# Kernel tuning notes

Measured on AMD Instinct MI355X. Metric: run time of the kernel, lower is better.

## Reference

```python
import jax, jax.numpy as jnp
import numpy as np

N_GRAPHS = 512
NODES_PER_G = 200
EDGES_PER_G = 6400
N = N_GRAPHS * NODES_PER_G        # 102400 nodes
E = N_GRAPHS * EDGES_PER_G        # 3276800 edges
HID = 128
NCLS = 10


def _linear_params(key, fan_in, fan_out):
    # torch nn.Linear default init: U(-1/sqrt(fan_in), 1/sqrt(fan_in))
    s = 1.0 / np.sqrt(fan_in)
    kw, kb = jax.random.split(key)
    W = jax.random.uniform(kw, (fan_in, fan_out), minval=-s, maxval=s, dtype=jnp.float32)
    b = jax.random.uniform(kb, (fan_out,), minval=-s, maxval=s, dtype=jnp.float32)
    return W, b


def setup_inputs() -> dict:
    key = jax.random.key(0)
    ks = jax.random.split(key, 10)
    # edges are confined within each graph (DGL batched graph structure)
    g_off = (jnp.arange(E, dtype=jnp.int32) // EDGES_PER_G) * NODES_PER_G
    src = (g_off + jax.random.randint(ks[0], (E,), 0, NODES_PER_G)).astype(jnp.int32)
    dst = (g_off + jax.random.randint(ks[1], (E,), 0, NODES_PER_G)).astype(jnp.int32)
    W1, b1 = _linear_params(ks[2], 1, HID)
    W2, b2 = _linear_params(ks[3], HID, HID)
    Wa, ba = _linear_params(ks[4], HID, 512)
    Wb, bb = _linear_params(ks[5], 512, 1024)
    Wc, bc = _linear_params(ks[6], 1024, 1024)
    Wd, bd = _linear_params(ks[7], 1024, 512)
    We, be = _linear_params(ks[8], 512, NCLS)
    return dict(src=src, dst=dst, W1=W1, b1=b1, W2=W2, b2=b2,
                Wa=Wa, ba=ba, Wb=Wb, bb=bb, Wc=Wc, bc=bc,
                Wd=Wd, bd=bd, We=We, be=be)


def reference(src, dst, W1, b1, W2, b2, Wa, ba, Wb, bb, Wc, bc, Wd, bd, We, be):
    seg = jax.ops.segment_sum
    ones = jnp.ones((E,), jnp.float32)
    in_deg = seg(ones, dst, num_segments=N)    # [N]
    out_deg = seg(ones, src, num_segments=N)   # [N]
    # DGL GraphConv norm='both': degrees clamped to min 1
    inv_out = (1.0 / jnp.sqrt(jnp.maximum(out_deg, 1.0)))[:, None]
    inv_in = (1.0 / jnp.sqrt(jnp.maximum(in_deg, 1.0)))[:, None]

    def gconv(h, W, b):
        h = (h @ W) * inv_out                    # src-side normalize (weight applied first; same math)
        h = seg(h[src], dst, num_segments=N)     # gather + scatter-add aggregation
        return h * inv_in + b                    # dst-side normalize + bias

    h = in_deg[:, None]                          # input node features = in-degrees, [N,1]
    h = jax.nn.relu(gconv(h, W1, b1))
    h = jax.nn.relu(gconv(h, W2, b2))

    gid = jnp.arange(N, dtype=jnp.int32) // NODES_PER_G
    hg = seg(h, gid, num_segments=N_GRAPHS) / float(NODES_PER_G)  # mean readout, [G,HID]

    x = jax.nn.relu(hg @ Wa + ba)
    x = jax.nn.relu(x @ Wb + bb)
    x = jax.nn.relu(x @ Wc + bc)
    x = jax.nn.relu(x @ Wd + bd)
    return jax.nn.softmax(x @ We + be, axis=-1)  # nn.Softmax over class dim
```

## Files before the change

kernel.cpp:

```cpp
#include <hip/hip_runtime.h>
#include <stdint.h>

typedef unsigned short u16;
typedef unsigned int   u32;

#define NG   512
#define NPG  200
#define EPG  6400
#define NN   (NG*NPG)
#define NE_  (NG*EPG)
#define HID  128
#define KP   224
#define AP   232
#define ZP   136
#define RQ   64
#define QCAP 2048

__device__ __forceinline__ float bf2f(u16 b){ u32 u = ((u32)b) << 16; return __builtin_bit_cast(float, u); }
__device__ __forceinline__ u16 f2bf(float f){
    u32 u = __builtin_bit_cast(u32, f);
    u = (u + 0x7FFFu + ((u >> 16) & 1u)) >> 16;
    return (u16)u;
}

typedef __attribute__((ext_vector_type(8))) short bf16x8;
typedef __attribute__((ext_vector_type(4))) float f32x4;

enum : int {
  O_W1 = 0,        O_b1 = 128,      O_W2 = 256,      O_b2 = 16640,
  O_Wa = 16768,    O_ba = 82304,    O_Wb = 82816,    O_bb = 607104,
  O_Wc = 608128,   O_bc = 1656704,  O_Wd = 1657728,  O_bd = 2182016,
  O_We = 2182528,  O_be = 2187648,  O_END = 2187658
};

enum : int {
  T_Wa = 0,
  T_Wb = 65536,
  T_Wc = 65536 + 524288,
  T_Wd = 65536 + 524288 + 1048576,
  T_END = 65536 + 524288 + 1048576 + 524288
};

__global__ __launch_bounds__(128) void k_detect(const u16* __restrict__ w1bits,
                                                int* __restrict__ flag)
{
    __shared__ int cnt;
    const int tid = threadIdx.x;
    if (tid == 0) cnt = 0;
    __syncthreads();
    u16 u = w1bits[tid];
    int e = (u >> 7) & 0xFF;
    if (e >= 0x7F) atomicAdd(&cnt, 1);
    __syncthreads();
    if (tid == 0) *flag = (cnt > 4) ? 1 : 0;
}

struct Cvt { const void* src[14]; int off[15]; };

__global__ __launch_bounds__(256) void k_convert(Cvt c, float* __restrict__ dst,
                                                 const int* __restrict__ flag, int total)
{
    const int f = *flag;
    int i = blockIdx.x * 256 + threadIdx.x;
    if (i >= total) return;
    int t = 0;
    while (i >= c.off[t+1]) t++;
    int j = i - c.off[t];
    dst[i] = f ? ((const float*)c.src[t])[j] : bf2f(((const u16*)c.src[t])[j]);
}

__global__ __launch_bounds__(256) void k_w2t(const void* __restrict__ w2src,
                                             const float* __restrict__ w2canon,
                                             u16* __restrict__ W2T,
                                             float* __restrict__ hg,
                                             const int* __restrict__ flag)
{
    int i = blockIdx.x * 256 + threadIdx.x;
    if (i < HID*HID){
        int outc = i >> 7, inc = i & 127;
        int jsrc = inc*HID + outc;
        W2T[i] = (*flag) ? f2bf(w2canon[jsrc]) : ((const u16*)w2src)[jsrc];
    }
    #pragma unroll
    for (int k = 0; k < 4; k++){
        int j = blockIdx.x * 1024 + k*256 + threadIdx.x;
        if (j < NG*HID) hg[j] = 0.f;
    }
}

struct TD { const void* src; int coff; int logK; int N; int dst0; int dst1; };
struct TD4 { TD t[4]; };

__global__ __launch_bounds__(256) void k_wt(TD4 d, const float* __restrict__ canon,
                                            u16* __restrict__ dst,
                                            const int* __restrict__ flag, int total)
{
    const int f = *flag;
    int i = blockIdx.x * 256 + threadIdx.x;
    if (i >= total) return;
    int t = 0;
    while (i >= d.t[t].dst1) t++;
    const TD& td = d.t[t];
    int j = i - td.dst0;
    int n = j >> td.logK;
    int k = j & ((1 << td.logK) - 1);
    int srcidx = k * td.N + n;
    dst[i] = f ? f2bf(canon[td.coff + srcidx]) : ((const u16*)td.src)[srcidx];
}

__global__ __launch_bounds__(256) void k_graph_l1(
    const int* __restrict__ src, const int* __restrict__ dst,
    const float* __restrict__ W1, const float* __restrict__ b1,
    float* __restrict__ invInG, u16* __restrict__ h1sT,
    u32* __restrict__ edgeBuf, int* __restrict__ cntQ)
{
    __shared__ u16 srcL[EPG];
    __shared__ u16 dstL[EPG];
    __shared__ int degIn[NPG];
    __shared__ int degOut[NPG];
    __shared__ int qcur[4];
    __shared__ float sValL[NPG], sAgg[NPG], iiL[NPG], ioL[NPG], tL[NPG];
    __shared__ float w1L[HID], b1L[HID];

    const int g = blockIdx.x, tid = threadIdx.x;

    if (tid < NPG){ degIn[tid] = 0; degOut[tid] = 0; sAgg[tid] = 0.f; }
    if (tid < HID){ w1L[tid] = W1[tid]; b1L[tid] = b1[tid]; }
    if (tid < 4) qcur[tid] = 0;
    __syncthreads();

    const int ebase = g * EPG;
    #pragma unroll
    for (int i = 0; i < EPG/256; i++){
        int e = i*256 + tid;
        int s = src[ebase + e] - g*NPG;
        int d = dst[ebase + e] - g*NPG;
        srcL[e] = (u16)s; dstL[e] = (u16)d;
        atomicAdd(&degOut[s], 1);
        atomicAdd(&degIn[d], 1);
    }
    __syncthreads();

    if (tid < NPG){
        int din = degIn[tid], dout = degOut[tid];
        float ii = rsqrtf(fmaxf((float)din, 1.f));
        float io = rsqrtf(fmaxf((float)dout, 1.f));
        iiL[tid] = ii; ioL[tid] = io;
        sValL[tid] = (float)din * io;
        invInG[g*NPG + tid] = ii;
    }
    __syncthreads();

    #pragma unroll
    for (int i = 0; i < EPG/256; i++){
        int e = i*256 + tid;
        int s = srcL[e], d = dstL[e];
        atomicAdd(&sAgg[d], sValL[s]);
        int q = (d * 41) >> 11;
        int pos = atomicAdd(&qcur[q], 1);
        if (pos < QCAP)
            edgeBuf[((size_t)(g*4 + q))*QCAP + pos] = (u32)s | ((u32)(d - q*50) << 16);
    }
    __syncthreads();

    if (tid < 4) cntQ[g*4 + tid] = (qcur[tid] < QCAP) ? qcur[tid] : QCAP;
    if (tid < NPG) tL[tid] = sAgg[tid] * iiL[tid];
    __syncthreads();

    const size_t base = (size_t)g * HID * KP;
    #pragma unroll 4
    for (int i = 0; i < HID*KP/256; i++){
        int idx = i*256 + tid;
        int c = idx / KP, v = idx - c*KP;
        u16 o = 0;
        if (v < NPG)
            o = f2bf(fmaxf(fmaf(tL[v], w1L[c], b1L[c]), 0.f) * ioL[v]);
        h1sT[base + idx] = o;
    }
}

__global__ __launch_bounds__(256, 4) void k_fused_graph(
    const u32* __restrict__ edgeBuf, const int* __restrict__ cntQ,
    const u16* __restrict__ h1sT, const u16* __restrict__ W2T,
    const float* __restrict__ invInG, const float* __restrict__ b2,
    float* __restrict__ hg)
{
    __shared__ __align__(16) u16 AZ[RQ*AP];
    __shared__ float invInL[RQ];
    __shared__ float b2L[HID];
    __shared__ float poolL[HID];

    const int bid = blockIdx.x, tid = threadIdx.x;
    const int g = bid >> 2, q = bid & 3;
    u32* az32 = (u32*)AZ;
    uint4* az4 = (uint4*)AZ;

    #pragma unroll
    for (int i = 0; i < 8; i++){
        int idx = i*256 + tid;
        if (idx < RQ*AP/8) az4[idx] = make_uint4(0,0,0,0);
    }
    if (tid < HID){ b2L[tid] = b2[tid]; poolL[tid] = 0.f; }
    if (tid < RQ) invInL[tid] = (tid < 50) ? invInG[g*NPG + q*50 + tid] : 0.f;
    __syncthreads();

    const int cnt = cntQ[bid];
    const u32* eb = edgeBuf + (size_t)bid * QCAP;
    for (int i = tid; i < cnt; i += 256){
        u32 e = eb[i];
        int s = e & 0xFFFF, dl = e >> 16;
        int idx = dl*AP + s;
        atomicAdd(&az32[idx >> 1], 1u << (16*(idx & 1)));
    }
    __syncthreads();

    for (int i = tid; i < RQ*AP/2; i += 256){
        u32 wv = az32[i];
        if (wv)
            az32[i] = (u32)f2bf((float)(wv & 0xFFFFu)) | ((u32)f2bf((float)(wv >> 16)) << 16);
    }
    __syncthreads();

    const int w = tid >> 6, lane = tid & 63;
    const int wm = w >> 1, wn = w & 1;
    const int lr = lane & 15, quad = lane >> 4;

    f32x4 acc[2][4];
    const f32x4 fz = {0.f, 0.f, 0.f, 0.f};
    #pragma unroll
    for (int mi = 0; mi < 2; mi++)
        #pragma unroll
        for (int nt = 0; nt < 4; nt++) acc[mi][nt] = fz;

    {
        const u16* Bg = h1sT + (size_t)g * HID * KP + (size_t)(wn*64) * KP;
        bf16x8 bcur[4], bnxt[4];
        #pragma unroll
        for (int nt = 0; nt < 4; nt++)
            bcur[nt] = *(const bf16x8*)&Bg[(nt*16 + lr)*KP + quad*8];
        for (int ks = 0; ks < 7; ks++){
            if (ks < 6){
                #pragma unroll
                for (int nt = 0; nt < 4; nt++)
                    bnxt[nt] = *(const bf16x8*)&Bg[(nt*16 + lr)*KP + (ks+1)*32 + quad*8];
            }
            bf16x8 af[2];
            #pragma unroll
            for (int mi = 0; mi < 2; mi++)
                af[mi] = *(const bf16x8*)&AZ[((wm*2 + mi)*16 + lr)*AP + ks*32 + quad*8];
            #pragma unroll
            for (int mi = 0; mi < 2; mi++)
                #pragma unroll
                for (int nt = 0; nt < 4; nt++)
                    acc[mi][nt] = __builtin_amdgcn_mfma_f32_16x16x32_bf16(
                        af[mi], bcur[nt], acc[mi][nt], 0, 0, 0);
            #pragma unroll
            for (int nt = 0; nt < 4; nt++) bcur[nt] = bnxt[nt];
        }
    }
    __syncthreads();

    #pragma unroll
    for (int mi = 0; mi < 2; mi++)
        #pragma unroll
        for (int nt = 0; nt < 4; nt++)
            #pragma unroll
            for (int r = 0; r < 4; r++){
                int v = (wm*2 + mi)*16 + quad*4 + r;
                int c = wn*64 + nt*16 + lr;
                AZ[v*ZP + c] = f2bf(acc[mi][nt][r]);
            }
    __syncthreads();

    #pragma unroll
    for (int mi = 0; mi < 2; mi++)
        #pragma unroll
        for (int nt = 0; nt < 4; nt++) acc[mi][nt] = fz;
    {
        const u16* Wg = W2T + (size_t)(wn*64) * HID;
        bf16x8 bcur[4], bnxt[4];
        #pragma unroll
        for (int nt = 0; nt < 4; nt++)
            bcur[nt] = *(const bf16x8*)&Wg[(nt*16 + lr)*HID + quad*8];
        for (int ks = 0; ks < 4; ks++){
            if (ks < 3){
                #pragma unroll
                for (int nt = 0; nt < 4; nt++)
                    bnxt[nt] = *(const bf16x8*)&Wg[(nt*16 + lr)*HID + (ks+1)*32 + quad*8];
            }
            bf16x8 af[2];
            #pragma unroll
            for (int mi = 0; mi < 2; mi++)
                af[mi] = *(const bf16x8*)&AZ[((wm*2 + mi)*16 + lr)*ZP + ks*32 + quad*8];
            #pragma unroll
            for (int mi = 0; mi < 2; mi++)
                #pragma unroll
                for (int nt = 0; nt < 4; nt++)
                    acc[mi][nt] = __builtin_amdgcn_mfma_f32_16x16x32_bf16(
                        af[mi], bcur[nt], acc[mi][nt], 0, 0, 0);
            #pragma unroll
            for (int nt = 0; nt < 4; nt++) bcur[nt] = bnxt[nt];
        }
    }

    #pragma unroll
    for (int mi = 0; mi < 2; mi++)
        #pragma unroll
        for (int nt = 0; nt < 4; nt++){
            int c = wn*64 + nt*16 + lr;
            float s = 0.f;
            #pragma unroll
            for (int r = 0; r < 4; r++){
                int v = (wm*2 + mi)*16 + quad*4 + r;
                if (v < 50)
                    s += fmaxf(fmaf(acc[mi][nt][r], invInL[v], b2L[c]), 0.f);
            }
            atomicAdd(&poolL[c], s);
        }
    __syncthreads();
    if (tid < HID) atomicAdd(&hg[(size_t)g*HID + tid], poolL[tid] * (1.f / NPG));
}

template<int K, bool AF32>
__global__ __launch_bounds__(512) void k_mlp3(
    const void* __restrict__ Ahi_, const u16* __restrict__ Alo,
    const u16* __restrict__ WT, const float* __restrict__ bias,
    u16* __restrict__ Ohi, u16* __restrict__ Olo, int Nc)
{
    __shared__ float red[32][68];

    const int tid = threadIdx.x;
    const int w = tid >> 6, lane = tid & 63;
    const int kz = w >> 2, wm = (w >> 1) & 1, wn = w & 1;
    const int lr = lane & 15, quad = lane >> 4;
    const int row0 = blockIdx.x * 32, col0 = blockIdx.y * 64;
    const int m = row0 + wm*16 + lr;
    constexpr int KH = K / 2;
    const int k0 = kz * KH;

    const float* Af = (const float*)Ahi_;
    const u16*   Ah = (const u16*)Ahi_;

    const f32x4 fz = {0.f, 0.f, 0.f, 0.f};
    f32x4 acc[2] = {fz, fz};

    #pragma unroll
    for (int ks = 0; ks < KH/32; ks++){
        const int kk = k0 + ks*32 + quad*8;
        bf16x8 ahi, alo;
        if constexpr (AF32){
            float xs[8];
            *(float4*)&xs[0] = *(const float4*)&Af[(size_t)m*K + kk];
            *(float4*)&xs[4] = *(const float4*)&Af[(size_t)m*K + kk + 4];
            #pragma unroll
            for (int j = 0; j < 8; j++){
                u16 hh = f2bf(xs[j]);
                ahi[j] = (short)hh;
                alo[j] = (short)f2bf(xs[j] - bf2f(hh));
            }
        } else {
            ahi = *(const bf16x8*)&Ah[(size_t)m*K + kk];
            alo = *(const bf16x8*)&Alo[(size_t)m*K + kk];
        }
        #pragma unroll
        for (int nt = 0; nt < 2; nt++){
            int n = col0 + wn*32 + nt*16 + lr;
            bf16x8 b = *(const bf16x8*)&WT[(size_t)n*K + kk];
            acc[nt] = __builtin_amdgcn_mfma_f32_16x16x32_bf16(ahi, b, acc[nt], 0, 0, 0);
            acc[nt] = __builtin_amdgcn_mfma_f32_16x16x32_bf16(alo, b, acc[nt], 0, 0, 0);
        }
    }

    if (kz == 1){
        #pragma unroll
        for (int nt = 0; nt < 2; nt++)
            #pragma unroll
            for (int r = 0; r < 4; r++)
                red[wm*16 + quad*4 + r][wn*32 + nt*16 + lr] = acc[nt][r];
    }
    __syncthreads();
    if (kz == 0){
        #pragma unroll
        for (int nt = 0; nt < 2; nt++)
            #pragma unroll
            for (int r = 0; r < 4; r++){
                int rr = wm*16 + quad*4 + r;
                int cc = wn*32 + nt*16 + lr;
                float v = acc[nt][r] + red[rr][cc] + bias[col0 + cc];
                v = fmaxf(v, 0.f);
                u16 hh = f2bf(v);
                size_t go = (size_t)(row0 + rr) * Nc + col0 + cc;
                Ohi[go] = hh;
                Olo[go] = f2bf(v - bf2f(hh));
            }
    }
}

__global__ __launch_bounds__(64) void k_head(
    const u16* __restrict__ Xhi, const u16* __restrict__ Xlo,
    const float* __restrict__ We, const float* __restrict__ be,
    void* __restrict__ out, const int* __restrict__ flag)
{
    const int g = blockIdx.x, lane = threadIdx.x;
    float part[10];
    #pragma unroll
    for (int c = 0; c < 10; c++) part[c] = 0.f;
    for (int k = lane; k < 512; k += 64){
        float x = bf2f(Xhi[(size_t)g*512 + k]) + bf2f(Xlo[(size_t)g*512 + k]);
        #pragma unroll
        for (int c = 0; c < 10; c++) part[c] = fmaf(x, We[k*10 + c], part[c]);
    }
    #pragma unroll
    for (int c = 0; c < 10; c++){
        float v = part[c];
        for (int off = 32; off > 0; off >>= 1) v += __shfl_down(v, off);
        part[c] = v;
    }
    if (lane == 0){
        const int f = *flag;
        #pragma unroll
        for (int c = 0; c < 10; c++) part[c] += be[c];
        float m = part[0];
        #pragma unroll
        for (int c = 1; c < 10; c++) m = fmaxf(m, part[c]);
        float e[10], s = 0.f;
        #pragma unroll
        for (int c = 0; c < 10; c++){ e[c] = __expf(part[c] - m); s += e[c]; }
        float inv = 1.f / s;
        #pragma unroll
        for (int c = 0; c < 10; c++){
            float p = e[c] * inv;
            if (f) ((float*)out)[g*10 + c] = p;
            else   ((u16*)out)[g*10 + c]  = f2bf(p);
        }
    }
}

extern "C" void kernel_launch(void* const* d_in, const int* in_sizes, int n_in,
                              void* d_out, int out_size, void* d_ws, size_t ws_size,
                              hipStream_t stream)
{
    const int* src = (const int*)d_in[0];
    const int* dst = (const int*)d_in[1];

    char* ws = (char*)d_ws;
    size_t o = 0;
    int*   flag     = (int*)  (ws + o); o += 16;
    float* wcanon   = (float*)(ws + o); o += ((size_t)O_END * 4 + 15) & ~(size_t)15;
    u16*   W2T      = (u16*)  (ws + o); o += (size_t)HID * HID * 2;
    u16*   WTa      = (u16*)  (ws + o); o += ((size_t)T_END * 2 + 15) & ~(size_t)15;
    float* invIn    = (float*)(ws + o); o += (size_t)NN * 4;
    u32*   edgeBuf  = (u32*)  (ws + o); o += (size_t)NG * 4 * QCAP * 4;
    int*   cntQ     = (int*)  (ws + o); o += (size_t)NG * 4 * 4;
    u16*   h1sT     = (u16*)  (ws + o); o += (size_t)NG * HID * KP * 2;
    float* hg       = (float*)(ws + o); o += (size_t)NG * HID * 4;
    u16*   X1hi     = (u16*)  (ws + o); o += (size_t)NG * 512 * 2;
    u16*   X1lo     = (u16*)  (ws + o); o += (size_t)NG * 512 * 2;
    u16*   X2hi     = (u16*)  (ws + o); o += (size_t)NG * 1024 * 2;
    u16*   X2lo     = (u16*)  (ws + o); o += (size_t)NG * 1024 * 2;
    u16*   X3hi     = (u16*)  (ws + o); o += (size_t)NG * 1024 * 2;
    u16*   X3lo     = (u16*)  (ws + o); o += (size_t)NG * 1024 * 2;
    u16*   X4hi     = (u16*)  (ws + o); o += (size_t)NG * 512 * 2;
    u16*   X4lo     = (u16*)  (ws + o); o += (size_t)NG * 512 * 2;
    (void)ws_size; (void)in_sizes; (void)n_in; (void)out_size;

    k_detect<<<dim3(1), dim3(128), 0, stream>>>((const u16*)d_in[2], flag);

    Cvt cv;
    const int offs[15] = {O_W1,O_b1,O_W2,O_b2,O_Wa,O_ba,O_Wb,O_bb,O_Wc,O_bc,O_Wd,O_bd,O_We,O_be,O_END};
    for (int i = 0; i < 14; i++){ cv.src[i] = d_in[2 + i]; cv.off[i] = offs[i]; }
    cv.off[14] = offs[14];
    k_convert<<<dim3((O_END + 255)/256), dim3(256), 0, stream>>>(cv, wcanon, flag, O_END);
    k_w2t<<<dim3(64), dim3(256), 0, stream>>>(d_in[4], wcanon + O_W2, W2T, hg, flag);

    TD4 td;
    td.t[0] = { d_in[6],  O_Wa, 7,  512,  T_Wa, T_Wb };
    td.t[1] = { d_in[8],  O_Wb, 9,  1024, T_Wb, T_Wc };
    td.t[2] = { d_in[10], O_Wc, 10, 1024, T_Wc, T_Wd };
    td.t[3] = { d_in[12], O_Wd, 10, 512,  T_Wd, T_END };
    k_wt<<<dim3((T_END + 255)/256), dim3(256), 0, stream>>>(td, wcanon, WTa, flag, T_END);

    const float *W1 = wcanon+O_W1, *b1 = wcanon+O_b1, *b2 = wcanon+O_b2;
    const float *ba = wcanon+O_ba, *bb = wcanon+O_bb, *bc = wcanon+O_bc, *bd = wcanon+O_bd;
    const float *We = wcanon+O_We, *be = wcanon+O_be;

    k_graph_l1<<<dim3(NG), dim3(256), 0, stream>>>(
        src, dst, W1, b1, invIn, h1sT, edgeBuf, cntQ);

    k_fused_graph<<<dim3(NG*4), dim3(256), 0, stream>>>(
        edgeBuf, cntQ, h1sT, W2T, invIn, b2, hg);

    k_mlp3<128,  true ><<<dim3(16, 8),  dim3(512), 0, stream>>>(hg,   nullptr, WTa + T_Wa, ba, X1hi, X1lo, 512);
    k_mlp3<512,  false><<<dim3(16, 16), dim3(512), 0, stream>>>(X1hi, X1lo,    WTa + T_Wb, bb, X2hi, X2lo, 1024);
    k_mlp3<1024, false><<<dim3(16, 16), dim3(512), 0, stream>>>(X2hi, X2lo,    WTa + T_Wc, bc, X3hi, X3lo, 1024);
    k_mlp3<1024, false><<<dim3(16, 8),  dim3(512), 0, stream>>>(X3hi, X3lo,    WTa + T_Wd, bd, X4hi, X4lo, 512);

    k_head<<<dim3(NG), dim3(64), 0, stream>>>(X4hi, X4lo, We, be, d_out, flag);
}
```

Before: 278.8 us.

## Merge prep kernels, build dense adjacency in global memory, pipeline MLP loads

```diff
diff --git a/kernel.cpp b/kernel.cpp
--- a/kernel.cpp
+++ b/kernel.cpp
@@ -11,10 +11,10 @@
 #define NE_  (NG*EPG)
 #define HID  128
 #define KP   224
-#define AP   232
+#define AW   224
+#define AG   57344
 #define ZP   136
 #define RQ   64
-#define QCAP 2048
 
 __device__ __forceinline__ float bf2f(u16 b){ u32 u = ((u32)b) << 16; return __builtin_bit_cast(float, u); }
 __device__ __forceinline__ u16 f2bf(float f){
@@ -26,99 +26,70 @@
 typedef __attribute__((ext_vector_type(8))) short bf16x8;
 typedef __attribute__((ext_vector_type(4))) float f32x4;
 
-enum : int {
-  O_W1 = 0,        O_b1 = 128,      O_W2 = 256,      O_b2 = 16640,
-  O_Wa = 16768,    O_ba = 82304,    O_Wb = 82816,    O_bb = 607104,
-  O_Wc = 608128,   O_bc = 1656704,  O_Wd = 1657728,  O_bd = 2182016,
-  O_We = 2182528,  O_be = 2187648,  O_END = 2187658
-};
-
-enum : int {
-  T_Wa = 0,
-  T_Wb = 65536,
-  T_Wc = 65536 + 524288,
-  T_Wd = 65536 + 524288 + 1048576,
-  T_END = 65536 + 524288 + 1048576 + 524288
-};
-
-__global__ __launch_bounds__(128) void k_detect(const u16* __restrict__ w1bits,
-                                                int* __restrict__ flag)
-{
-    __shared__ int cnt;
+enum : int { cW1=0, cb1=128, cb2=256, cba=384, cbb=896, cbc=1920, cbd=2944, cWe=3456, cbe=8576, cEND=8586 };
+enum : int { T_Wa=0, T_Wb=65536, T_Wc=589824, T_Wd=1638400, T_END=2162688 };
+enum : int { B0=8586, B1=24970, B2=2187658, B3=2253194 };
+
+struct PrepIn { const void* p[14]; };
+
+__global__ __launch_bounds__(256) void k_prep(PrepIn in, float* __restrict__ canon,
+                                              u16* __restrict__ W2T, u16* __restrict__ WTa,
+                                              float* __restrict__ hg)
+{
+    __shared__ int sflag;
     const int tid = threadIdx.x;
-    if (tid == 0) cnt = 0;
-    __syncthreads();
-    u16 u = w1bits[tid];
-    int e = (u >> 7) & 0xFF;
-    if (e >= 0x7F) atomicAdd(&cnt, 1);
-    __syncthreads();
-    if (tid == 0) *flag = (cnt > 4) ? 1 : 0;
-}
-
-struct Cvt { const void* src[14]; int off[15]; };
-
-__global__ __launch_bounds__(256) void k_convert(Cvt c, float* __restrict__ dst,
-                                                 const int* __restrict__ flag, int total)
-{
-    const int f = *flag;
-    int i = blockIdx.x * 256 + threadIdx.x;
-    if (i >= total) return;
-    int t = 0;
-    while (i >= c.off[t+1]) t++;
-    int j = i - c.off[t];
-    dst[i] = f ? ((const float*)c.src[t])[j] : bf2f(((const u16*)c.src[t])[j]);
-}
-
-__global__ __launch_bounds__(256) void k_w2t(const void* __restrict__ w2src,
-                                             const float* __restrict__ w2canon,
-                                             u16* __restrict__ W2T,
-                                             float* __restrict__ hg,
-                                             const int* __restrict__ flag)
-{
-    int i = blockIdx.x * 256 + threadIdx.x;
-    if (i < HID*HID){
-        int outc = i >> 7, inc = i & 127;
-        int jsrc = inc*HID + outc;
-        W2T[i] = (*flag) ? f2bf(w2canon[jsrc]) : ((const u16*)w2src)[jsrc];
-    }
-    #pragma unroll
-    for (int k = 0; k < 4; k++){
-        int j = blockIdx.x * 1024 + k*256 + threadIdx.x;
-        if (j < NG*HID) hg[j] = 0.f;
-    }
-}
-
-struct TD { const void* src; int coff; int logK; int N; int dst0; int dst1; };
-struct TD4 { TD t[4]; };
-
-__global__ __launch_bounds__(256) void k_wt(TD4 d, const float* __restrict__ canon,
-                                            u16* __restrict__ dst,
-                                            const int* __restrict__ flag, int total)
-{
-    const int f = *flag;
-    int i = blockIdx.x * 256 + threadIdx.x;
-    if (i >= total) return;
-    int t = 0;
-    while (i >= d.t[t].dst1) t++;
-    const TD& td = d.t[t];
-    int j = i - td.dst0;
-    int n = j >> td.logK;
-    int k = j & ((1 << td.logK) - 1);
-    int srcidx = k * td.N + n;
-    dst[i] = f ? f2bf(canon[td.coff + srcidx]) : ((const u16*)td.src)[srcidx];
+    if (tid < 64){
+        const u16* wb = (const u16*)in.p[0];
+        u16 a = wb[tid], b = wb[64 + tid];
+        unsigned long long m1 = __ballot((int)((a >> 7) & 0xFF) >= 0x7F);
+        unsigned long long m2 = __ballot((int)((b >> 7) & 0xFF) >= 0x7F);
+        if (tid == 0) sflag = (__popcll(m1) + __popcll(m2) > 4) ? 1 : 0;
+    }
+    __syncthreads();
+    const int f = sflag;
+
+    int i = blockIdx.x * 256 + tid;
+    if (i >= B3) return;
+
+    if (i < B0){
+        const void* s; int off;
+        if      (i < 128) { s = in.p[0];  off = i; }
+        else if (i < 256) { s = in.p[1];  off = i - 128; }
+        else if (i < 384) { s = in.p[3];  off = i - 256; }
+        else if (i < 896) { s = in.p[5];  off = i - 384; }
+        else if (i < 1920){ s = in.p[7];  off = i - 896; }
+        else if (i < 2944){ s = in.p[9];  off = i - 1920; }
+        else if (i < 3456){ s = in.p[11]; off = i - 2944; }
+        else if (i < 8576){ s = in.p[12]; off = i - 3456; }
+        else              { s = in.p[13]; off = i - 8576; }
+        canon[i] = f ? ((const float*)s)[off] : bf2f(((const u16*)s)[off]);
+    } else if (i < B1){
+        int j = i - B0;
+        int outc = j >> 7, inc = j & 127;
+        int si = inc * HID + outc;
+        W2T[j] = f ? f2bf(((const float*)in.p[2])[si]) : ((const u16*)in.p[2])[si];
+    } else if (i < B2){
+        int j = i - B1;
+        const void* s; int si;
+        if (j < T_Wb){ s = in.p[4];  int n = j >> 7,  k = j & 127;  si = k*512  + n; }
+        else if (j < T_Wc){ int jj = j - T_Wb; s = in.p[6];  int n = jj >> 9,  k = jj & 511;  si = k*1024 + n; }
+        else if (j < T_Wd){ int jj = j - T_Wc; s = in.p[8];  int n = jj >> 10, k = jj & 1023; si = k*1024 + n; }
+        else              { int jj = j - T_Wd; s = in.p[10]; int n = jj >> 10, k = jj & 1023; si = k*512  + n; }
+        WTa[j] = f ? f2bf(((const float*)s)[si]) : ((const u16*)s)[si];
+    } else {
+        hg[i - B2] = 0.f;
+    }
 }
 
 __global__ __launch_bounds__(256) void k_graph_l1(
     const int* __restrict__ src, const int* __restrict__ dst,
     const float* __restrict__ W1, const float* __restrict__ b1,
-    float* __restrict__ invInG, u16* __restrict__ h1sT,
-    u32* __restrict__ edgeBuf, int* __restrict__ cntQ)
+    float* __restrict__ invInG, u16* __restrict__ h1sT)
 {
     __shared__ u16 srcL[EPG];
     __shared__ u16 dstL[EPG];
     __shared__ int degIn[NPG];
     __shared__ int degOut[NPG];
-    __shared__ int qcur[4];
     __shared__ float sValL[NPG], sAgg[NPG], iiL[NPG], ioL[NPG], tL[NPG];
     __shared__ float w1L[HID], b1L[HID];
 
@@ -126,7 +97,6 @@
 
     if (tid < NPG){ degIn[tid] = 0; degOut[tid] = 0; sAgg[tid] = 0.f; }
     if (tid < HID){ w1L[tid] = W1[tid]; b1L[tid] = b1[tid]; }
-    if (tid < 4) qcur[tid] = 0;
     __syncthreads();
 
     const int ebase = g * EPG;
@@ -154,16 +124,10 @@
     #pragma unroll
     for (int i = 0; i < EPG/256; i++){
         int e = i*256 + tid;
-        int s = srcL[e], d = dstL[e];
-        atomicAdd(&sAgg[d], sValL[s]);
-        int q = (d * 41) >> 11;
-        int pos = atomicAdd(&qcur[q], 1);
-        if (pos < QCAP)
-            edgeBuf[((size_t)(g*4 + q))*QCAP + pos] = (u32)s | ((u32)(d - q*50) << 16);
-    }
-    __syncthreads();
-
-    if (tid < 4) cntQ[g*4 + tid] = (qcur[tid] < QCAP) ? qcur[tid] : QCAP;
+        atomicAdd(&sAgg[dstL[e]], sValL[srcL[e]]);
+    }
+    __syncthreads();
+
     if (tid < NPG) tL[tid] = sAgg[tid] * iiL[tid];
     __syncthreads();
 
@@ -179,47 +143,63 @@
     }
 }
 
-__global__ __launch_bounds__(256, 4) void k_fused_graph(
-    const u32* __restrict__ edgeBuf, const int* __restrict__ cntQ,
+__global__ __launch_bounds__(256) void k_buildA(
+    const int* __restrict__ src, const int* __restrict__ dst,
+    u16* __restrict__ Adense)
+{
+    __shared__ u32 A32[AG/2];
+    const int g = blockIdx.x, tid = threadIdx.x;
+
+    uint4* a4 = (uint4*)A32;
+    #pragma unroll
+    for (int i = 0; i < AG/8/256; i++)
+        a4[i*256 + tid] = make_uint4(0,0,0,0);
+    __syncthreads();
+
+    const int ebase = g * EPG;
+    #pragma unroll
+    for (int i = 0; i < EPG/256; i++){
+        int e = i*256 + tid;
+        int s = src[ebase + e] - g*NPG;
+        int d = dst[ebase + e] - g*NPG;
+        int q = (d * 41) >> 11;
+        int idx = (q*64 + (d - q*50))*AW + s;
+        atomicAdd(&A32[idx >> 1], 1u << (16*(idx & 1)));
+    }
+    __syncthreads();
+
+    uint4* g4 = (uint4*)(Adense + (size_t)g * AG);
+    #pragma unroll 4
+    for (int i = 0; i < AG/8/256; i++){
+        uint4 v = a4[i*256 + tid];
+        u32* pv = (u32*)&v;
+        #pragma unroll
+        for (int j = 0; j < 4; j++){
+            u32 wv = pv[j];
+            pv[j] = (u32)f2bf((float)(wv & 0xFFFFu)) | ((u32)f2bf((float)(wv >> 16)) << 16);
+        }
+        g4[i*256 + tid] = v;
+    }
+}
+
+__global__ __launch_bounds__(256, 5) void k_fused_graph(
+    const u16* __restrict__ Adense,
     const u16* __restrict__ h1sT, const u16* __restrict__ W2T,
     const float* __restrict__ invInG, const float* __restrict__ b2,
     float* __restrict__ hg)
 {
-    __shared__ __align__(16) u16 AZ[RQ*AP];
+    __shared__ __align__(16) u16 Zs[RQ*ZP];
     __shared__ float invInL[RQ];
     __shared__ float b2L[HID];
     __shared__ float poolL[HID];
 
     const int bid = blockIdx.x, tid = threadIdx.x;
-    const int g = bid >> 2, q = bid & 3;
-    u32* az32 = (u32*)AZ;
-    uint4* az4 = (uint4*)AZ;
-
-    #pragma unroll
-    for (int i = 0; i < 8; i++){
-        int idx = i*256 + tid;
-        if (idx < RQ*AP/8) az4[idx] = make_uint4(0,0,0,0);
-    }
+    const int xcd = bid & 7, slot = bid >> 3;
+    const int g = (slot >> 2) * 8 + xcd;
+    const int q = slot & 3;
+
     if (tid < HID){ b2L[tid] = b2[tid]; poolL[tid] = 0.f; }
     if (tid < RQ) invInL[tid] = (tid < 50) ? invInG[g*NPG + q*50 + tid] : 0.f;
-    __syncthreads();
-
-    const int cnt = cntQ[bid];
-    const u32* eb = edgeBuf + (size_t)bid * QCAP;
-    for (int i = tid; i < cnt; i += 256){
-        u32 e = eb[i];
-        int s = e & 0xFFFF, dl = e >> 16;
-        int idx = dl*AP + s;
-        atomicAdd(&az32[idx >> 1], 1u << (16*(idx & 1)));
-    }
-    __syncthreads();
-
-    for (int i = tid; i < RQ*AP/2; i += 256){
-        u32 wv = az32[i];
-        if (wv)
-            az32[i] = (u32)f2bf((float)(wv & 0xFFFFu)) | ((u32)f2bf((float)(wv >> 16)) << 16);
-    }
-    __syncthreads();
 
     const int w = tid >> 6, lane = tid & 63;
     const int wm = w >> 1, wn = w & 1;
@@ -233,32 +213,36 @@
         for (int nt = 0; nt < 4; nt++) acc[mi][nt] = fz;
 
     {
+        const u16* Ag = Adense + (size_t)g * AG + (size_t)q * 64 * AW;
         const u16* Bg = h1sT + (size_t)g * HID * KP + (size_t)(wn*64) * KP;
-        bf16x8 bcur[4], bnxt[4];
+        bf16x8 bcur[4], bnxt[4], acur[2], anxt[2];
         #pragma unroll
         for (int nt = 0; nt < 4; nt++)
             bcur[nt] = *(const bf16x8*)&Bg[(nt*16 + lr)*KP + quad*8];
+        #pragma unroll
+        for (int mi = 0; mi < 2; mi++)
+            acur[mi] = *(const bf16x8*)&Ag[((wm*2 + mi)*16 + lr)*AW + quad*8];
         for (int ks = 0; ks < 7; ks++){
             if (ks < 6){
                 #pragma unroll
                 for (int nt = 0; nt < 4; nt++)
                     bnxt[nt] = *(const bf16x8*)&Bg[(nt*16 + lr)*KP + (ks+1)*32 + quad*8];
-            }
-            bf16x8 af[2];
-            #pragma unroll
-            for (int mi = 0; mi < 2; mi++)
-                af[mi] = *(const bf16x8*)&AZ[((wm*2 + mi)*16 + lr)*AP + ks*32 + quad*8];
+                #pragma unroll
+                for (int mi = 0; mi < 2; mi++)
+                    anxt[mi] = *(const bf16x8*)&Ag[((wm*2 + mi)*16 + lr)*AW + (ks+1)*32 + quad*8];
+            }
             #pragma unroll
             for (int mi = 0; mi < 2; mi++)
                 #pragma unroll
                 for (int nt = 0; nt < 4; nt++)
                     acc[mi][nt] = __builtin_amdgcn_mfma_f32_16x16x32_bf16(
-                        af[mi], bcur[nt], acc[mi][nt], 0, 0, 0);
+                        acur[mi], bcur[nt], acc[mi][nt], 0, 0, 0);
             #pragma unroll
             for (int nt = 0; nt < 4; nt++) bcur[nt] = bnxt[nt];
-        }
-    }
-    __syncthreads();
+            #pragma unroll
+            for (int mi = 0; mi < 2; mi++) acur[mi] = anxt[mi];
+        }
+    }
 
     #pragma unroll
     for (int mi = 0; mi < 2; mi++)
@@ -268,7 +252,7 @@
             for (int r = 0; r < 4; r++){
                 int v = (wm*2 + mi)*16 + quad*4 + r;
                 int c = wn*64 + nt*16 + lr;
-                AZ[v*ZP + c] = f2bf(acc[mi][nt][r]);
+                Zs[v*ZP + c] = f2bf(acc[mi][nt][r]);
             }
     __syncthreads();
 
@@ -291,7 +275,7 @@
             bf16x8 af[2];
             #pragma unroll
             for (int mi = 0; mi < 2; mi++)
-                af[mi] = *(const bf16x8*)&AZ[((wm*2 + mi)*16 + lr)*ZP + ks*32 + quad*8];
+                af[mi] = *(const bf16x8*)&Zs[((wm*2 + mi)*16 + lr)*ZP + ks*32 + quad*8];
             #pragma unroll
             for (int mi = 0; mi < 2; mi++)
                 #pragma unroll
@@ -322,12 +306,13 @@
 }
 
 template<int K, bool AF32>
-__global__ __launch_bounds__(512) void k_mlp3(
+__global__ __launch_bounds__(512) void k_mlp5(
     const void* __restrict__ Ahi_, const u16* __restrict__ Alo,
     const u16* __restrict__ WT, const float* __restrict__ bias,
     u16* __restrict__ Ohi, u16* __restrict__ Olo, int Nc)
 {
-    __shared__ float red[32][68];
+    constexpr int ITERS = K / 64;
+    __shared__ __align__(16) float red[32][68];
 
     const int tid = threadIdx.x;
     const int w = tid >> 6, lane = tid & 63;
@@ -335,19 +320,13 @@
     const int lr = lane & 15, quad = lane >> 4;
     const int row0 = blockIdx.x * 32, col0 = blockIdx.y * 64;
     const int m = row0 + wm*16 + lr;
-    constexpr int KH = K / 2;
-    const int k0 = kz * KH;
+    const int k0 = kz * (K/2);
 
     const float* Af = (const float*)Ahi_;
     const u16*   Ah = (const u16*)Ahi_;
 
-    const f32x4 fz = {0.f, 0.f, 0.f, 0.f};
-    f32x4 acc[2] = {fz, fz};
-
-    #pragma unroll
-    for (int ks = 0; ks < KH/32; ks++){
-        const int kk = k0 + ks*32 + quad*8;
-        bf16x8 ahi, alo;
+    auto loadA = [&](int it, bf16x8& hi, bf16x8& lo){
+        const int kk = k0 + it*32 + quad*8;
         if constexpr (AF32){
             float xs[8];
             *(float4*)&xs[0] = *(const float4*)&Af[(size_t)m*K + kk];
@@ -355,20 +334,36 @@
             #pragma unroll
             for (int j = 0; j < 8; j++){
                 u16 hh = f2bf(xs[j]);
-                ahi[j] = (short)hh;
-                alo[j] = (short)f2bf(xs[j] - bf2f(hh));
+                hi[j] = (short)hh;
+                lo[j] = (short)f2bf(xs[j] - bf2f(hh));
             }
         } else {
-            ahi = *(const bf16x8*)&Ah[(size_t)m*K + kk];
-            alo = *(const bf16x8*)&Alo[(size_t)m*K + kk];
-        }
+            hi = *(const bf16x8*)&Ah[(size_t)m*K + kk];
+            lo = *(const bf16x8*)&Alo[(size_t)m*K + kk];
+        }
+    };
+    auto loadB = [&](int it, bf16x8* b){
+        const int kk = k0 + it*32 + quad*8;
         #pragma unroll
         for (int nt = 0; nt < 2; nt++){
             int n = col0 + wn*32 + nt*16 + lr;
-            bf16x8 b = *(const bf16x8*)&WT[(size_t)n*K + kk];
-            acc[nt] = __builtin_amdgcn_mfma_f32_16x16x32_bf16(ahi, b, acc[nt], 0, 0, 0);
-            acc[nt] = __builtin_amdgcn_mfma_f32_16x16x32_bf16(alo, b, acc[nt], 0, 0, 0);
-        }
+            b[nt] = *(const bf16x8*)&WT[(size_t)n*K + kk];
+        }
+    };
+
+    const f32x4 fz = {0.f, 0.f, 0.f, 0.f};
+    f32x4 acc[2] = {fz, fz};
+    bf16x8 chi, clo, cb[2], nhi, nlo, nb[2];
+    loadA(0, chi, clo); loadB(0, cb);
+    #pragma unroll 2
+    for (int it = 0; it < ITERS; it++){
+        if (it + 1 < ITERS){ loadA(it+1, nhi, nlo); loadB(it+1, nb); }
+        #pragma unroll
+        for (int nt = 0; nt < 2; nt++){
+            acc[nt] = __builtin_amdgcn_mfma_f32_16x16x32_bf16(chi, cb[nt], acc[nt], 0, 0, 0);
+            acc[nt] = __builtin_amdgcn_mfma_f32_16x16x32_bf16(clo, cb[nt], acc[nt], 0, 0, 0);
+        }
+        chi = nhi; clo = nlo; cb[0] = nb[0]; cb[1] = nb[1];
     }
 
     if (kz == 1){
@@ -399,9 +394,14 @@
 __global__ __launch_bounds__(64) void k_head(
     const u16* __restrict__ Xhi, const u16* __restrict__ Xlo,
     const float* __restrict__ We, const float* __restrict__ be,
-    void* __restrict__ out, const int* __restrict__ flag)
+    void* __restrict__ out, const u16* __restrict__ w1bits)
 {
     const int g = blockIdx.x, lane = threadIdx.x;
+    u16 a = w1bits[lane], b = w1bits[64 + lane];
+    unsigned long long m1 = __ballot((int)((a >> 7) & 0xFF) >= 0x7F);
+    unsigned long long m2 = __ballot((int)((b >> 7) & 0xFF) >= 0x7F);
+    const int f = (__popcll(m1) + __popcll(m2) > 4) ? 1 : 0;
+
     float part[10];
     #pragma unroll
     for (int c = 0; c < 10; c++) part[c] = 0.f;
@@ -417,7 +417,6 @@
         part[c] = v;
     }
     if (lane == 0){
-        const int f = *flag;
         #pragma unroll
         for (int c = 0; c < 10; c++) part[c] += be[c];
         float m = part[0];
@@ -445,13 +444,11 @@
 
     char* ws = (char*)d_ws;
     size_t o = 0;
-    int*   flag     = (int*)  (ws + o); o += 16;
-    float* wcanon   = (float*)(ws + o); o += ((size_t)O_END * 4 + 15) & ~(size_t)15;
+    float* canon    = (float*)(ws + o); o += ((size_t)cEND * 4 + 15) & ~(size_t)15;
     u16*   W2T      = (u16*)  (ws + o); o += (size_t)HID * HID * 2;
     u16*   WTa      = (u16*)  (ws + o); o += ((size_t)T_END * 2 + 15) & ~(size_t)15;
     float* invIn    = (float*)(ws + o); o += (size_t)NN * 4;
-    u32*   edgeBuf  = (u32*)  (ws + o); o += (size_t)NG * 4 * QCAP * 4;
-    int*   cntQ     = (int*)  (ws + o); o += (size_t)NG * 4 * 4;
+    u16*   Adense   = (u16*)  (ws + o); o += (size_t)NG * AG * 2;
     u16*   h1sT     = (u16*)  (ws + o); o += (size_t)NG * HID * KP * 2;
     float* hg       = (float*)(ws + o); o += (size_t)NG * HID * 4;
     u16*   X1hi     = (u16*)  (ws + o); o += (size_t)NG * 512 * 2;
@@ -464,36 +461,26 @@
     u16*   X4lo     = (u16*)  (ws + o); o += (size_t)NG * 512 * 2;
     (void)ws_size; (void)in_sizes; (void)n_in; (void)out_size;
 
-    k_detect<<<dim3(1), dim3(128), 0, stream>>>((const u16*)d_in[2], flag);
-
-    Cvt cv;
-    const int offs[15] = {O_W1,O_b1,O_W2,O_b2,O_Wa,O_ba,O_Wb,O_bb,O_Wc,O_bc,O_Wd,O_bd,O_We,O_be,O_END};
-    for (int i = 0; i < 14; i++){ cv.src[i] = d_in[2 + i]; cv.off[i] = offs[i]; }
-    cv.off[14] = offs[14];
-    k_convert<<<dim3((O_END + 255)/256), dim3(256), 0, stream>>>(cv, wcanon, flag, O_END);
-    k_w2t<<<dim3(64), dim3(256), 0, stream>>>(d_in[4], wcanon + O_W2, W2T, hg, flag);
-
-    TD4 td;
-    td.t[0] = { d_in[6],  O_Wa, 7,  512,  T_Wa, T_Wb };
-    td.t[1] = { d_in[8],  O_Wb, 9,  1024, T_Wb, T_Wc };
-    td.t[2] = { d_in[10], O_Wc, 10, 1024, T_Wc, T_Wd };
-    td.t[3] = { d_in[12], O_Wd, 10, 512,  T_Wd, T_END };
-    k_wt<<<dim3((T_END + 255)/256), dim3(256), 0, stream>>>(td, wcanon, WTa, flag, T_END);
-
-    const float *W1 = wcanon+O_W1, *b1 = wcanon+O_b1, *b2 = wcanon+O_b2;
-    const float *ba = wcanon+O_ba, *bb = wcanon+O_bb, *bc = wcanon+O_bc, *bd = wcanon+O_bd;
-    const float *We = wcanon+O_We, *be = wcanon+O_be;
+    PrepIn pin;
+    for (int i = 0; i < 14; i++) pin.p[i] = d_in[2 + i];
+    k_prep<<<dim3((B3 + 255)/256), dim3(256), 0, stream>>>(pin, canon, W2T, WTa, hg);
+
+    const float *W1 = canon+cW1, *b1 = canon+cb1, *b2 = canon+cb2;
+    const float *ba = canon+cba, *bb = canon+cbb, *bc = canon+cbc, *bd = canon+cbd;
+    const float *We = canon+cWe, *be = canon+cbe;
 
     k_graph_l1<<<dim3(NG), dim3(256), 0, stream>>>(
-        src, dst, W1, b1, invIn, h1sT, edgeBuf, cntQ);
+        src, dst, W1, b1, invIn, h1sT);
+
+    k_buildA<<<dim3(NG), dim3(256), 0, stream>>>(src, dst, Adense);
 
     k_fused_graph<<<dim3(NG*4), dim3(256), 0, stream>>>(
-        edgeBuf, cntQ, h1sT, W2T, invIn, b2, hg);
-
-    k_mlp3<128,  true ><<<dim3(16, 8),  dim3(512), 0, stream>>>(hg,   nullptr, WTa + T_Wa, ba, X1hi, X1lo, 512);
-    k_mlp3<512,  false><<<dim3(16, 16), dim3(512), 0, stream>>>(X1hi, X1lo,    WTa + T_Wb, bb, X2hi, X2lo, 1024);
-    k_mlp3<1024, false><<<dim3(16, 16), dim3(512), 0, stream>>>(X2hi, X2lo,    WTa + T_Wc, bc, X3hi, X3lo, 1024);
-    k_mlp3<1024, false><<<dim3(16, 8),  dim3(512), 0, stream>>>(X3hi, X3lo,    WTa + T_Wd, bd, X4hi, X4lo, 512);
-
-    k_head<<<dim3(NG), dim3(64), 0, stream>>>(X4hi, X4lo, We, be, d_out, flag);
-}
+        Adense, h1sT, W2T, invIn, b2, hg);
+
+    k_mlp5<128,  true ><<<dim3(16, 8),  dim3(512), 0, stream>>>(hg,   nullptr, WTa + T_Wa, ba, X1hi, X1lo, 512);
+    k_mlp5<512,  false><<<dim3(16, 16), dim3(512), 0, stream>>>(X1hi, X1lo,    WTa + T_Wb, bb, X2hi, X2lo, 1024);
+    k_mlp5<1024, false><<<dim3(16, 16), dim3(512), 0, stream>>>(X2hi, X2lo,    WTa + T_Wc, bc, X3hi, X3lo, 1024);
+    k_mlp5<1024, false><<<dim3(16, 8),  dim3(512), 0, stream>>>(X3hi, X3lo,    WTa + T_Wd, bd, X4hi, X4lo, 512);
+
+    k_head<<<dim3(NG), dim3(64), 0, stream>>>(X4hi, X4lo, We, be, d_out, (const u16*)d_in[2]);
+}
```

After: 283.7 us. Within noise of the previous version (+1.8%).
